# Kernel tuning notes

Hardware: AMD Instinct MI355X
Metric: run time of the kernel (lower is better)

## Reference

```python
import jax, jax.numpy as jnp
import numpy as np

EPS = 1e-7
MAX_TANH = 1.0 - 1e-6  # clamp for arctanh stability


def _norm(v):
    # last-axis L2 norm, clamped away from zero
    return jnp.maximum(jnp.linalg.norm(v, axis=-1, keepdims=True), EPS)


def log_map_zero(y):
    # Poincare ball (c=1) log map at the origin
    n = _norm(y)
    return jnp.arctanh(jnp.clip(n, 0.0, MAX_TANH)) * y / n


def exp_map_zero(v):
    # Poincare ball (c=1) exp map at the origin
    n = _norm(v)
    return jnp.tanh(n) * v / n


def h_add(x, y):
    # Mobius addition x (+) y on the Poincare ball (c=1)
    xy = jnp.sum(x * y, axis=-1, keepdims=True)
    x2 = jnp.sum(x * x, axis=-1, keepdims=True)
    y2 = jnp.sum(y * y, axis=-1, keepdims=True)
    num = (1.0 + 2.0 * xy + y2) * x + (1.0 - x2) * y
    den = 1.0 + 2.0 * xy + x2 * y2
    return num / jnp.maximum(den, EPS)


def h_mul(x, W):
    # Mobius matrix-vector multiply: exp0( log0(x) @ W )
    return exp_map_zero(log_map_zero(x) @ W)


def setup_inputs() -> dict:
    key = jax.random.key(0)
    k1, k2, k3, k4 = jax.random.split(key, 4)
    N, F_IN, F_OUT = 8192, 128, 128
    # node features inside the unit ball: ||x|| ~ 0.05*sqrt(128) ~ 0.57
    x = 0.05 * jax.random.normal(k1, (N, F_IN), dtype=jnp.float32)
    # sparse-ish row-normalized dense adjacency
    a = (jax.random.uniform(k2, (N, N)) < 0.01).astype(jnp.float32)
    adj = a / jnp.maximum(a.sum(axis=1, keepdims=True), 1.0)
    # xavier-uniform-ish weights
    lim_e = np.sqrt(6.0 / (F_IN + F_IN)) * np.sqrt(2.0)
    lim_l = np.sqrt(6.0 / (2 * F_IN + F_OUT)) * np.sqrt(2.0)
    embed = jax.random.uniform(k3, (F_IN, F_IN), minval=-lim_e, maxval=lim_e, dtype=jnp.float32)
    layer = jax.random.uniform(k4, (2 * F_IN, F_OUT), minval=-lim_l, maxval=lim_l, dtype=jnp.float32)
    embed_bias = jnp.zeros((F_IN,), dtype=jnp.float32)
    layer_bias = jnp.zeros((F_OUT,), dtype=jnp.float32)
    return {"x": x, "adj": adj, "embed": embed, "layer": layer,
            "embed_bias": embed_bias, "layer_bias": layer_bias}


def reference(x, adj, embed, layer, embed_bias, layer_bias):
    # h = (embed (x)mobius x) (+) embed_bias
    h = h_mul(x, embed)                      # [N, F_IN]
    h = h_add(h, embed_bias[None, :])
    # neighbor aggregation in tangent space at origin
    neigh = exp_map_zero(adj @ log_map_zero(h))   # [N, F_IN]
    # out = (layer (x)mobius [x ; neigh]) (+) layer_bias
    out = h_mul(jnp.concatenate((x, neigh), axis=1), layer)  # [N, F_OUT]
    out = h_add(out, layer_bias[None, :])
    return out
```

## Files before the change

kernel.cpp:

```cpp
#include <hip/hip_runtime.h>
#include <math.h>

#define EPS  1e-7f
#define MAXT 0.999999f

typedef short  s16x8  __attribute__((ext_vector_type(8)));
typedef float  f32x16 __attribute__((ext_vector_type(16)));

__device__ __forceinline__ float waveRedSum(float v) {
    #pragma unroll
    for (int off = 32; off > 0; off >>= 1)
        v += __shfl_xor(v, off, 64);
    return v;
}

__device__ __forceinline__ unsigned short f2bf(float f) {
    unsigned u = __float_as_uint(f);
    u += 0x7fff + ((u >> 16) & 1);
    return (unsigned short)(u >> 16);
}

__global__ __launch_bounds__(256) void kA(const float* __restrict__ x,
                                          const float* __restrict__ embed,
                                          const float* __restrict__ ebias,
                                          unsigned short* __restrict__ vpack) {
    __shared__ float u[4][128];
    const int wave = threadIdx.x >> 6;
    const int lane = threadIdx.x & 63;
    const int row  = blockIdx.x * 4 + wave;
    const int c0   = lane * 2;

    const float2 xr = *(const float2*)(x + (size_t)row * 128 + c0);

    float n2 = waveRedSum(xr.x * xr.x + xr.y * xr.y);
    float n  = fmaxf(sqrtf(n2), EPS);
    float sc = atanhf(fminf(n, MAXT)) / n;
    u[wave][c0]     = xr.x * sc;
    u[wave][c0 + 1] = xr.y * sc;
    __syncthreads();

    float a0 = 0.f, a1 = 0.f;
    #pragma unroll 8
    for (int k = 0; k < 128; k++) {
        float  uk = u[wave][k];
        float2 e  = *(const float2*)(embed + (size_t)k * 128 + c0);
        a0 = fmaf(uk, e.x, a0);
        a1 = fmaf(uk, e.y, a1);
    }

    float np2 = waveRedSum(a0 * a0 + a1 * a1);
    float np  = fmaxf(sqrtf(np2), EPS);
    float se  = tanhf(np) / np;
    float h0 = a0 * se, h1 = a1 * se;
    float x2 = np2 * se * se;

    float bx = ebias[c0], by = ebias[c0 + 1];
    float xy = waveRedSum(h0 * bx + h1 * by);
    float y2 = waveRedSum(bx * bx + by * by);
    float den = fmaxf(1.f + 2.f * xy + x2 * y2, EPS);
    float cx = 1.f + 2.f * xy + y2;
    float cy = 1.f - x2;
    float hb0 = (cx * h0 + cy * bx) / den;
    float hb1 = (cx * h1 + cy * by) / den;

    float m2 = waveRedSum(hb0 * hb0 + hb1 * hb1);
    float m  = fmaxf(sqrtf(m2), EPS);
    float sl = atanhf(fminf(m, MAXT)) / m;
    float v0 = hb0 * sl, v1 = hb1 * sl;

    const int tbase = (row >> 4) * 2048 + (row & 15);
    vpack[tbase + c0 * 16]       = f2bf(v0);
    vpack[tbase + (c0 + 1) * 16] = f2bf(v1);
}

#define BK 128

__global__ __launch_bounds__(256) void kB(const float* __restrict__ adj,
                                          const unsigned short* __restrict__ vpack,
                                          float* __restrict__ tpart,
                                          int klen) {
    __shared__ __align__(16) unsigned short As[32][BK + 8];

    const int tid  = threadIdx.x;
    const int wave = tid >> 6;
    const int lane = tid & 63;
    const int r0   = blockIdx.x * 32;
    const int k0   = blockIdx.y * klen;
    float* tout    = tpart + (size_t)blockIdx.y * 8192 * 128;

    const int srow = tid >> 3;
    const int scol = (tid & 7) * 16;
    const float* aptr = adj + (size_t)(r0 + srow) * 8192 + k0 + scol;

    const int m  = lane & 31;
    const int kh = lane >> 5;
    const int n  = wave * 32 + m;
    const unsigned short* vb = vpack + (size_t)n * 16 + kh * 8;

    f32x16 acc = {0.f};

    float4 f0 = *(const float4*)(aptr + 0);
    float4 f1 = *(const float4*)(aptr + 4);
    float4 f2 = *(const float4*)(aptr + 8);
    float4 f3 = *(const float4*)(aptr + 12);

    const int kiters = klen / BK;
    for (int it = 0; it < kiters; it++) {
        __syncthreads();

        union { unsigned short u[8]; s16x8 v; } p0, p1;
        p0.u[0] = f2bf(f0.x); p0.u[1] = f2bf(f0.y); p0.u[2] = f2bf(f0.z); p0.u[3] = f2bf(f0.w);
        p0.u[4] = f2bf(f1.x); p0.u[5] = f2bf(f1.y); p0.u[6] = f2bf(f1.z); p0.u[7] = f2bf(f1.w);
        p1.u[0] = f2bf(f2.x); p1.u[1] = f2bf(f2.y); p1.u[2] = f2bf(f2.z); p1.u[3] = f2bf(f2.w);
        p1.u[4] = f2bf(f3.x); p1.u[5] = f2bf(f3.y); p1.u[6] = f2bf(f3.z); p1.u[7] = f2bf(f3.w);
        *(s16x8*)&As[srow][scol]     = p0.v;
        *(s16x8*)&As[srow][scol + 8] = p1.v;
        __syncthreads();

        if (it + 1 < kiters) {
            aptr += BK;
            f0 = *(const float4*)(aptr + 0);
            f1 = *(const float4*)(aptr + 4);
            f2 = *(const float4*)(aptr + 8);
            f3 = *(const float4*)(aptr + 12);
        }

        const int ktile0 = (k0 + it * BK) >> 4;
        #pragma unroll
        for (int kk = 0; kk < BK / 16; kk++) {
            s16x8 a = *(const s16x8*)&As[m][kk * 16 + kh * 8];
            s16x8 b = *(const s16x8*)(vb + (size_t)(ktile0 + kk) * 2048);
            acc = __builtin_amdgcn_mfma_f32_32x32x16_bf16(a, b, acc, 0, 0, 0);
        }
    }

    #pragma unroll
    for (int r = 0; r < 16; r++) {
        int row = r0 + (r & 3) + 8 * (r >> 2) + 4 * kh;
        tout[(size_t)row * 128 + n] = acc[r];
    }
}

__global__ __launch_bounds__(256) void kC(const float* __restrict__ x,
                                          const float* __restrict__ tpart,
                                          const float* __restrict__ layer,
                                          const float* __restrict__ lbias,
                                          float* __restrict__ out,
                                          int S) {
    __shared__ float w[4][256];
    const int wave = threadIdx.x >> 6;
    const int lane = threadIdx.x & 63;
    const int row  = blockIdx.x * 4 + wave;
    const int c0   = lane * 2;

    float2 tr = *(const float2*)(tpart + (size_t)row * 128 + c0);
    for (int s = 1; s < S; s++) {
        float2 p = *(const float2*)(tpart + (size_t)s * 8192 * 128 + (size_t)row * 128 + c0);
        tr.x += p.x; tr.y += p.y;
    }
    const float2 xr = *(const float2*)(x + (size_t)row * 128 + c0);

    float st = waveRedSum(tr.x * tr.x + tr.y * tr.y);
    float sx = waveRedSum(xr.x * xr.x + xr.y * xr.y);

    float nt = fmaxf(sqrtf(st), EPS);
    float se = tanhf(nt) / nt;

    float ncat2 = sx + st * se * se;
    float ncat  = fmaxf(sqrtf(ncat2), EPS);
    float sw    = atanhf(fminf(ncat, MAXT)) / ncat;
    w[wave][c0]           = xr.x * sw;
    w[wave][c0 + 1]       = xr.y * sw;
    w[wave][128 + c0]     = tr.x * se * sw;
    w[wave][128 + c0 + 1] = tr.y * se * sw;
    __syncthreads();

    float a0 = 0.f, a1 = 0.f;
    #pragma unroll 8
    for (int k = 0; k < 256; k++) {
        float  wk = w[wave][k];
        float2 e  = *(const float2*)(layer + (size_t)k * 128 + c0);
        a0 = fmaf(wk, e.x, a0);
        a1 = fmaf(wk, e.y, a1);
    }

    float np2 = waveRedSum(a0 * a0 + a1 * a1);
    float np  = fmaxf(sqrtf(np2), EPS);
    float so  = tanhf(np) / np;
    float o0 = a0 * so, o1 = a1 * so;
    float x2 = np2 * so * so;

    float bx = lbias[c0], by = lbias[c0 + 1];
    float xy = waveRedSum(o0 * bx + o1 * by);
    float y2 = waveRedSum(bx * bx + by * by);
    float den = fmaxf(1.f + 2.f * xy + x2 * y2, EPS);
    float cx = 1.f + 2.f * xy + y2;
    float cy = 1.f - x2;

    float2 res;
    res.x = (cx * o0 + cy * bx) / den;
    res.y = (cx * o1 + cy * by) / den;
    *(float2*)(out + (size_t)row * 128 + c0) = res;
}

extern "C" void kernel_launch(void* const* d_in, const int* in_sizes, int n_in,
                              void* d_out, int out_size, void* d_ws, size_t ws_size,
                              hipStream_t stream) {
    const float* x     = (const float*)d_in[0];
    const float* adj   = (const float*)d_in[1];
    const float* embed = (const float*)d_in[2];
    const float* layer = (const float*)d_in[3];
    const float* eb    = (const float*)d_in[4];
    const float* lb    = (const float*)d_in[5];
    float* out = (float*)d_out;

    const size_t vbytes = (size_t)8192 * 128 * 2;
    const size_t slice  = (size_t)8192 * 128 * 4;

    int S = 1;
    if      (ws_size >= vbytes + 8 * slice) S = 8;
    else if (ws_size >= vbytes + 4 * slice) S = 4;
    else if (ws_size >= vbytes + 2 * slice) S = 2;

    unsigned short* vpack = (unsigned short*)d_ws;
    float* tpart = (float*)((char*)d_ws + vbytes);

    kA<<<2048, 256, 0, stream>>>(x, embed, eb, vpack);
    kB<<<dim3(256, S), 256, 0, stream>>>(adj, vpack, tpart, 8192 / S);
    kC<<<2048, 256, 0, stream>>>(x, tpart, layer, lb, out, S);
}
```

Baseline: 498.3 us.

## Fuse three stages into one cooperative persistent kernel with grid syncs

Replaces the three separate launches with a single cooperative kernel of 1024 blocks that runs the embed projection, the bf16 MFMA adjacency GEMM with a fixed 4-way K split, and the output projection, separated by grid-wide syncs. Each block processes two rows per wave in the elementwise stages so that embed and layer weight loads are reused. The aim is to remove launch gaps between stages. In exchange the GEMM has fewer K splits than the previous up-to-8, so less parallelism, and grid.sync carries its own overhead. A fallback to the old three-kernel path with S=8 runs if the cooperative launch fails; that fallback assumes the workspace holds 8 slices without checking ws_size.

Measured after the change: 709.8 us. 42.4% more time.

```diff
diff --git a/kernel.cpp b/kernel.cpp
--- a/kernel.cpp
+++ b/kernel.cpp
@@ -1,8 +1,11 @@
 #include <hip/hip_runtime.h>
+#include <hip/hip_cooperative_groups.h>
 #include <math.h>
 
 #define EPS  1e-7f
 #define MAXT 0.999999f
+
+namespace cg = cooperative_groups;
 
 typedef short  s16x8  __attribute__((ext_vector_type(8)));
 typedef float  f32x16 __attribute__((ext_vector_type(16)));
@@ -18,6 +21,196 @@
     unsigned u = __float_as_uint(f);
     u += 0x7fff + ((u >> 16) & 1);
     return (unsigned short)(u >> 16);
+}
+
+__device__ __forceinline__ void tangent_pack(float a0, float a1, float bx, float by,
+                                             float y2, int row, int c0,
+                                             unsigned short* __restrict__ vpack) {
+    float np2 = waveRedSum(a0*a0 + a1*a1);
+    float np  = fmaxf(sqrtf(np2), EPS);
+    float se  = tanhf(np)/np;
+    float h0 = a0*se, h1 = a1*se;
+    float x2 = np2*se*se;
+    float xy = waveRedSum(h0*bx + h1*by);
+    float den = fmaxf(1.f + 2.f*xy + x2*y2, EPS);
+    float cx = 1.f + 2.f*xy + y2;
+    float cy = 1.f - x2;
+    float hb0 = (cx*h0 + cy*bx)/den, hb1 = (cx*h1 + cy*by)/den;
+    float m2 = waveRedSum(hb0*hb0 + hb1*hb1);
+    float mm = fmaxf(sqrtf(m2), EPS);
+    float sl = atanhf(fminf(mm, MAXT))/mm;
+    const int tbase = (row >> 4)*2048 + (row & 15);
+    vpack[tbase + c0*16]       = f2bf(hb0*sl);
+    vpack[tbase + (c0+1)*16]   = f2bf(hb1*sl);
+}
+
+__device__ __forceinline__ void final_out(float a0, float a1, float bx, float by,
+                                          float y2, int row, int c0,
+                                          float* __restrict__ out) {
+    float np2 = waveRedSum(a0*a0 + a1*a1);
+    float np  = fmaxf(sqrtf(np2), EPS);
+    float so  = tanhf(np)/np;
+    float o0 = a0*so, o1 = a1*so;
+    float x2 = np2*so*so;
+    float xy = waveRedSum(o0*bx + o1*by);
+    float den = fmaxf(1.f + 2.f*xy + x2*y2, EPS);
+    float cx = 1.f + 2.f*xy + y2;
+    float cy = 1.f - x2;
+    float2 res;
+    res.x = (cx*o0 + cy*bx)/den;
+    res.y = (cx*o1 + cy*by)/den;
+    *(float2*)(out + (size_t)row*128 + c0) = res;
+}
+
+#define BK     128
+#define SPLITS 4
+#define KLEN   2048
+#define NBLK   1024
+
+__global__ __launch_bounds__(256, 4) void kFused(
+        const float* __restrict__ x, const float* __restrict__ adj,
+        const float* __restrict__ embed, const float* __restrict__ layer,
+        const float* __restrict__ eb, const float* __restrict__ lb,
+        float* __restrict__ out, unsigned short* __restrict__ vpack,
+        float* __restrict__ tpart)
+{
+    __shared__ __align__(16) char smraw[32*(BK+8)*2];
+    const int tid  = threadIdx.x;
+    const int wave = tid >> 6;
+    const int lane = tid & 63;
+    const int c0   = lane*2;
+    cg::grid_group grid = cg::this_grid();
+
+    {
+        float (*u)[2][128] = (float(*)[2][128])smraw;
+        const int row0 = blockIdx.x*8 + wave;
+        float2 xr0 = *(const float2*)(x + (size_t)row0*128 + c0);
+        float2 xr1 = *(const float2*)(x + (size_t)(row0+4)*128 + c0);
+        float n20 = waveRedSum(xr0.x*xr0.x + xr0.y*xr0.y);
+        float n21 = waveRedSum(xr1.x*xr1.x + xr1.y*xr1.y);
+        float nn0 = fmaxf(sqrtf(n20), EPS), nn1 = fmaxf(sqrtf(n21), EPS);
+        float s0 = atanhf(fminf(nn0, MAXT))/nn0;
+        float s1 = atanhf(fminf(nn1, MAXT))/nn1;
+        u[wave][0][c0] = xr0.x*s0; u[wave][0][c0+1] = xr0.y*s0;
+        u[wave][1][c0] = xr1.x*s1; u[wave][1][c0+1] = xr1.y*s1;
+        __syncthreads();
+        float a00=0.f, a01=0.f, a10=0.f, a11=0.f;
+        #pragma unroll 8
+        for (int k = 0; k < 128; k++) {
+            float uk0 = u[wave][0][k], uk1 = u[wave][1][k];
+            float2 e  = *(const float2*)(embed + (size_t)k*128 + c0);
+            a00 = fmaf(uk0, e.x, a00); a01 = fmaf(uk0, e.y, a01);
+            a10 = fmaf(uk1, e.x, a10); a11 = fmaf(uk1, e.y, a11);
+        }
+        float bx = eb[c0], by = eb[c0+1];
+        float y2 = waveRedSum(bx*bx + by*by);
+        tangent_pack(a00, a01, bx, by, y2, row0,     c0, vpack);
+        tangent_pack(a10, a11, bx, by, y2, row0 + 4, c0, vpack);
+    }
+
+    grid.sync();
+
+    {
+        unsigned short (*As)[BK+8] = (unsigned short(*)[BK+8])smraw;
+        const int bx = blockIdx.x & 255;
+        const int by = blockIdx.x >> 8;
+        const int r0 = bx*32;
+        const int k0 = by*KLEN;
+        float* tout  = tpart + (size_t)by * 8192 * 128;
+
+        const int srow = tid >> 3;
+        const int scol = (tid & 7) * 16;
+        const float* aptr = adj + (size_t)(r0 + srow)*8192 + k0 + scol;
+
+        const int m  = lane & 31;
+        const int kh = lane >> 5;
+        const int n  = wave*32 + m;
+        const unsigned short* vb = vpack + (size_t)n*16 + kh*8;
+
+        f32x16 acc = {0.f};
+
+        float4 f0 = *(const float4*)(aptr + 0);
+        float4 f1 = *(const float4*)(aptr + 4);
+        float4 f2 = *(const float4*)(aptr + 8);
+        float4 f3 = *(const float4*)(aptr + 12);
+
+        const int kiters = KLEN / BK;
+        for (int it = 0; it < kiters; it++) {
+            __syncthreads();
+            union { unsigned short u[8]; s16x8 v; } p0, p1;
+            p0.u[0]=f2bf(f0.x); p0.u[1]=f2bf(f0.y); p0.u[2]=f2bf(f0.z); p0.u[3]=f2bf(f0.w);
+            p0.u[4]=f2bf(f1.x); p0.u[5]=f2bf(f1.y); p0.u[6]=f2bf(f1.z); p0.u[7]=f2bf(f1.w);
+            p1.u[0]=f2bf(f2.x); p1.u[1]=f2bf(f2.y); p1.u[2]=f2bf(f2.z); p1.u[3]=f2bf(f2.w);
+            p1.u[4]=f2bf(f3.x); p1.u[5]=f2bf(f3.y); p1.u[6]=f2bf(f3.z); p1.u[7]=f2bf(f3.w);
+            *(s16x8*)&As[srow][scol]     = p0.v;
+            *(s16x8*)&As[srow][scol + 8] = p1.v;
+            __syncthreads();
+
+            if (it + 1 < kiters) {
+                aptr += BK;
+                f0 = *(const float4*)(aptr + 0);
+                f1 = *(const float4*)(aptr + 4);
+                f2 = *(const float4*)(aptr + 8);
+                f3 = *(const float4*)(aptr + 12);
+            }
+
+            const int ktile0 = (k0 + it*BK) >> 4;
+            #pragma unroll
+            for (int kk = 0; kk < BK/16; kk++) {
+                s16x8 a = *(const s16x8*)&As[m][kk*16 + kh*8];
+                s16x8 b = *(const s16x8*)(vb + (size_t)(ktile0 + kk)*2048);
+                acc = __builtin_amdgcn_mfma_f32_32x32x16_bf16(a, b, acc, 0, 0, 0);
+            }
+        }
+
+        #pragma unroll
+        for (int r = 0; r < 16; r++) {
+            int row = r0 + (r & 3) + 8*(r >> 2) + 4*kh;
+            tout[(size_t)row*128 + n] = acc[r];
+        }
+    }
+
+    grid.sync();
+
+    {
+        float (*w)[2][256] = (float(*)[2][256])smraw;
+        const int row0 = blockIdx.x*8 + wave;
+        #pragma unroll
+        for (int r = 0; r < 2; r++) {
+            const int row = row0 + 4*r;
+            float2 tr = *(const float2*)(tpart + (size_t)row*128 + c0);
+            #pragma unroll
+            for (int s = 1; s < SPLITS; s++) {
+                float2 p = *(const float2*)(tpart + (size_t)s*8192*128 + (size_t)row*128 + c0);
+                tr.x += p.x; tr.y += p.y;
+            }
+            const float2 xr = *(const float2*)(x + (size_t)row*128 + c0);
+            float st = waveRedSum(tr.x*tr.x + tr.y*tr.y);
+            float sx = waveRedSum(xr.x*xr.x + xr.y*xr.y);
+            float nt = fmaxf(sqrtf(st), EPS);
+            float se = tanhf(nt)/nt;
+            float ncat2 = sx + st*se*se;
+            float ncat  = fmaxf(sqrtf(ncat2), EPS);
+            float sw    = atanhf(fminf(ncat, MAXT))/ncat;
+            w[wave][r][c0]           = xr.x*sw;
+            w[wave][r][c0+1]         = xr.y*sw;
+            w[wave][r][128 + c0]     = tr.x*se*sw;
+            w[wave][r][128 + c0+1]   = tr.y*se*sw;
+        }
+        __syncthreads();
+        float a00=0.f, a01=0.f, a10=0.f, a11=0.f;
+        #pragma unroll 8
+        for (int k = 0; k < 256; k++) {
+            float wk0 = w[wave][0][k], wk1 = w[wave][1][k];
+            float2 e  = *(const float2*)(layer + (size_t)k*128 + c0);
+            a00 = fmaf(wk0, e.x, a00); a01 = fmaf(wk0, e.y, a01);
+            a10 = fmaf(wk1, e.x, a10); a11 = fmaf(wk1, e.y, a11);
+        }
+        float bx = lb[c0], by = lb[c0+1];
+        float y2 = waveRedSum(bx*bx + by*by);
+        final_out(a00, a01, bx, by, y2, row0,     c0, out);
+        final_out(a10, a11, bx, by, y2, row0 + 4, c0, out);
+    }
 }
 
 __global__ __launch_bounds__(256) void kA(const float* __restrict__ x,
@@ -31,7 +224,6 @@
     const int c0   = lane * 2;
 
     const float2 xr = *(const float2*)(x + (size_t)row * 128 + c0);
-
     float n2 = waveRedSum(xr.x * xr.x + xr.y * xr.y);
     float n  = fmaxf(sqrtf(n2), EPS);
     float sc = atanhf(fminf(n, MAXT)) / n;
@@ -47,40 +239,16 @@
         a0 = fmaf(uk, e.x, a0);
         a1 = fmaf(uk, e.y, a1);
     }
-
-    float np2 = waveRedSum(a0 * a0 + a1 * a1);
-    float np  = fmaxf(sqrtf(np2), EPS);
-    float se  = tanhf(np) / np;
-    float h0 = a0 * se, h1 = a1 * se;
-    float x2 = np2 * se * se;
-
     float bx = ebias[c0], by = ebias[c0 + 1];
-    float xy = waveRedSum(h0 * bx + h1 * by);
-    float y2 = waveRedSum(bx * bx + by * by);
-    float den = fmaxf(1.f + 2.f * xy + x2 * y2, EPS);
-    float cx = 1.f + 2.f * xy + y2;
-    float cy = 1.f - x2;
-    float hb0 = (cx * h0 + cy * bx) / den;
-    float hb1 = (cx * h1 + cy * by) / den;
-
-    float m2 = waveRedSum(hb0 * hb0 + hb1 * hb1);
-    float m  = fmaxf(sqrtf(m2), EPS);
-    float sl = atanhf(fminf(m, MAXT)) / m;
-    float v0 = hb0 * sl, v1 = hb1 * sl;
-
-    const int tbase = (row >> 4) * 2048 + (row & 15);
-    vpack[tbase + c0 * 16]       = f2bf(v0);
-    vpack[tbase + (c0 + 1) * 16] = f2bf(v1);
-}
-
-#define BK 128
+    float y2 = waveRedSum(bx*bx + by*by);
+    tangent_pack(a0, a1, bx, by, y2, row, c0, vpack);
+}
 
 __global__ __launch_bounds__(256) void kB(const float* __restrict__ adj,
                                           const unsigned short* __restrict__ vpack,
                                           float* __restrict__ tpart,
                                           int klen) {
     __shared__ __align__(16) unsigned short As[32][BK + 8];
-
     const int tid  = threadIdx.x;
     const int wave = tid >> 6;
     const int lane = tid & 63;
@@ -98,7 +266,6 @@
     const unsigned short* vb = vpack + (size_t)n * 16 + kh * 8;
 
     f32x16 acc = {0.f};
-
     float4 f0 = *(const float4*)(aptr + 0);
     float4 f1 = *(const float4*)(aptr + 4);
     float4 f2 = *(const float4*)(aptr + 8);
@@ -107,12 +274,11 @@
     const int kiters = klen / BK;
     for (int it = 0; it < kiters; it++) {
         __syncthreads();
-
         union { unsigned short u[8]; s16x8 v; } p0, p1;
-        p0.u[0] = f2bf(f0.x); p0.u[1] = f2bf(f0.y); p0.u[2] = f2bf(f0.z); p0.u[3] = f2bf(f0.w);
-        p0.u[4] = f2bf(f1.x); p0.u[5] = f2bf(f1.y); p0.u[6] = f2bf(f1.z); p0.u[7] = f2bf(f1.w);
-        p1.u[0] = f2bf(f2.x); p1.u[1] = f2bf(f2.y); p1.u[2] = f2bf(f2.z); p1.u[3] = f2bf(f2.w);
-        p1.u[4] = f2bf(f3.x); p1.u[5] = f2bf(f3.y); p1.u[6] = f2bf(f3.z); p1.u[7] = f2bf(f3.w);
+        p0.u[0]=f2bf(f0.x); p0.u[1]=f2bf(f0.y); p0.u[2]=f2bf(f0.z); p0.u[3]=f2bf(f0.w);
+        p0.u[4]=f2bf(f1.x); p0.u[5]=f2bf(f1.y); p0.u[6]=f2bf(f1.z); p0.u[7]=f2bf(f1.w);
+        p1.u[0]=f2bf(f2.x); p1.u[1]=f2bf(f2.y); p1.u[2]=f2bf(f2.z); p1.u[3]=f2bf(f2.w);
+        p1.u[4]=f2bf(f3.x); p1.u[5]=f2bf(f3.y); p1.u[6]=f2bf(f3.z); p1.u[7]=f2bf(f3.w);
         *(s16x8*)&As[srow][scol]     = p0.v;
         *(s16x8*)&As[srow][scol + 8] = p1.v;
         __syncthreads();
@@ -133,7 +299,6 @@
             acc = __builtin_amdgcn_mfma_f32_32x32x16_bf16(a, b, acc, 0, 0, 0);
         }
     }
-
     #pragma unroll
     for (int r = 0; r < 16; r++) {
         int row = r0 + (r & 3) + 8 * (r >> 2) + 4 * kh;
@@ -159,13 +324,10 @@
         tr.x += p.x; tr.y += p.y;
     }
     const float2 xr = *(const float2*)(x + (size_t)row * 128 + c0);
-
     float st = waveRedSum(tr.x * tr.x + tr.y * tr.y);
     float sx = waveRedSum(xr.x * xr.x + xr.y * xr.y);
-
     float nt = fmaxf(sqrtf(st), EPS);
     float se = tanhf(nt) / nt;
-
     float ncat2 = sx + st * se * se;
     float ncat  = fmaxf(sqrtf(ncat2), EPS);
     float sw    = atanhf(fminf(ncat, MAXT)) / ncat;
@@ -183,24 +345,9 @@
         a0 = fmaf(wk, e.x, a0);
         a1 = fmaf(wk, e.y, a1);
     }
-
-    float np2 = waveRedSum(a0 * a0 + a1 * a1);
-    float np  = fmaxf(sqrtf(np2), EPS);
-    float so  = tanhf(np) / np;
-    float o0 = a0 * so, o1 = a1 * so;
-    float x2 = np2 * so * so;
-
     float bx = lbias[c0], by = lbias[c0 + 1];
-    float xy = waveRedSum(o0 * bx + o1 * by);
     float y2 = waveRedSum(bx * bx + by * by);
-    float den = fmaxf(1.f + 2.f * xy + x2 * y2, EPS);
-    float cx = 1.f + 2.f * xy + y2;
-    float cy = 1.f - x2;
-
-    float2 res;
-    res.x = (cx * o0 + cy * bx) / den;
-    res.y = (cx * o1 + cy * by) / den;
-    *(float2*)(out + (size_t)row * 128 + c0) = res;
+    final_out(a0, a1, bx, by, y2, row, c0, out);
 }
 
 extern "C" void kernel_launch(void* const* d_in, const int* in_sizes, int n_in,
@@ -215,17 +362,18 @@
     float* out = (float*)d_out;
 
     const size_t vbytes = (size_t)8192 * 128 * 2;
-    const size_t slice  = (size_t)8192 * 128 * 4;
-
-    int S = 1;
-    if      (ws_size >= vbytes + 8 * slice) S = 8;
-    else if (ws_size >= vbytes + 4 * slice) S = 4;
-    else if (ws_size >= vbytes + 2 * slice) S = 2;
-
     unsigned short* vpack = (unsigned short*)d_ws;
     float* tpart = (float*)((char*)d_ws + vbytes);
 
-    kA<<<2048, 256, 0, stream>>>(x, embed, eb, vpack);
-    kB<<<dim3(256, S), 256, 0, stream>>>(adj, vpack, tpart, 8192 / S);
-    kC<<<2048, 256, 0, stream>>>(x, tpart, layer, lb, out, S);
-}
+    void* args[] = { (void*)&x, (void*)&adj, (void*)&embed, (void*)&layer,
+                     (void*)&eb, (void*)&lb, (void*)&out, (void*)&vpack, (void*)&tpart };
+
+    hipError_t err = hipLaunchCooperativeKernel(kFused, dim3(NBLK), dim3(256),
+                                                args, 0u, stream);
+    if (err != hipSuccess) {
+        const int S = 8;
+        kA<<<2048, 256, 0, stream>>>(x, embed, eb, vpack);
+        kB<<<dim3(256, S), 256, 0, stream>>>(adj, vpack, tpart, 8192 / S);
+        kC<<<2048, 256, 0, stream>>>(x, tpart, layer, lb, out, S);
+    }
+}
```

## Double-buffer adjacency tiles in LDS via async global-to-LDS copies

Applied to the files above, without the earlier changes.

The adjacency GEMM kernel now stages raw fp32 adj tiles into a double-buffered LDS array using global_load_lds async copies with an XOR swizzle. The next tile's copy is issued while MFMAs run on the current one, and bf16 conversion moves to the LDS read side. B fragments are prefetched into registers per iteration, launch bounds request 4 blocks per SM, and split-K is hardcoded to 8 regardless of workspace size. The remaining edits factor the epilogue math into helper functions. The change doubles LDS per block to 32KB, and forcing S=8 assumes the workspace is large enough.

Measured after the change: 488.9 us. Within noise of the previous version (-1.9%).

```diff
diff --git a/kernel.cpp b/kernel.cpp
--- a/kernel.cpp
+++ b/kernel.cpp
@@ -18,6 +18,52 @@
     unsigned u = __float_as_uint(f);
     u += 0x7fff + ((u >> 16) & 1);
     return (unsigned short)(u >> 16);
+}
+
+__device__ __forceinline__ void async_cp16(const float* src, void* ldsbase) {
+    __builtin_amdgcn_global_load_lds(
+        (const __attribute__((address_space(1))) unsigned int*)src,
+        (__attribute__((address_space(3))) unsigned int*)ldsbase,
+        16, 0, 0);
+}
+
+__device__ __forceinline__ void tangent_pack(float a0, float a1, float bx, float by,
+                                             float y2, int row, int c0,
+                                             unsigned short* __restrict__ vpack) {
+    float np2 = waveRedSum(a0*a0 + a1*a1);
+    float np  = fmaxf(sqrtf(np2), EPS);
+    float se  = tanhf(np)/np;
+    float h0 = a0*se, h1 = a1*se;
+    float x2 = np2*se*se;
+    float xy = waveRedSum(h0*bx + h1*by);
+    float den = fmaxf(1.f + 2.f*xy + x2*y2, EPS);
+    float cx = 1.f + 2.f*xy + y2;
+    float cy = 1.f - x2;
+    float hb0 = (cx*h0 + cy*bx)/den, hb1 = (cx*h1 + cy*by)/den;
+    float m2 = waveRedSum(hb0*hb0 + hb1*hb1);
+    float mm = fmaxf(sqrtf(m2), EPS);
+    float sl = atanhf(fminf(mm, MAXT))/mm;
+    const int tbase = (row >> 4)*2048 + (row & 15);
+    vpack[tbase + c0*16]       = f2bf(hb0*sl);
+    vpack[tbase + (c0+1)*16]   = f2bf(hb1*sl);
+}
+
+__device__ __forceinline__ void final_out(float a0, float a1, float bx, float by,
+                                          float y2, int row, int c0,
+                                          float* __restrict__ out) {
+    float np2 = waveRedSum(a0*a0 + a1*a1);
+    float np  = fmaxf(sqrtf(np2), EPS);
+    float so  = tanhf(np)/np;
+    float o0 = a0*so, o1 = a1*so;
+    float x2 = np2*so*so;
+    float xy = waveRedSum(o0*bx + o1*by);
+    float den = fmaxf(1.f + 2.f*xy + x2*y2, EPS);
+    float cx = 1.f + 2.f*xy + y2;
+    float cy = 1.f - x2;
+    float2 res;
+    res.x = (cx*o0 + cy*bx)/den;
+    res.y = (cx*o1 + cy*by)/den;
+    *(float2*)(out + (size_t)row*128 + c0) = res;
 }
 
 __global__ __launch_bounds__(256) void kA(const float* __restrict__ x,
@@ -31,7 +77,6 @@
     const int c0   = lane * 2;
 
     const float2 xr = *(const float2*)(x + (size_t)row * 128 + c0);
-
     float n2 = waveRedSum(xr.x * xr.x + xr.y * xr.y);
     float n  = fmaxf(sqrtf(n2), EPS);
     float sc = atanhf(fminf(n, MAXT)) / n;
@@ -47,40 +92,18 @@
         a0 = fmaf(uk, e.x, a0);
         a1 = fmaf(uk, e.y, a1);
     }
-
-    float np2 = waveRedSum(a0 * a0 + a1 * a1);
-    float np  = fmaxf(sqrtf(np2), EPS);
-    float se  = tanhf(np) / np;
-    float h0 = a0 * se, h1 = a1 * se;
-    float x2 = np2 * se * se;
-
     float bx = ebias[c0], by = ebias[c0 + 1];
-    float xy = waveRedSum(h0 * bx + h1 * by);
     float y2 = waveRedSum(bx * bx + by * by);
-    float den = fmaxf(1.f + 2.f * xy + x2 * y2, EPS);
-    float cx = 1.f + 2.f * xy + y2;
-    float cy = 1.f - x2;
-    float hb0 = (cx * h0 + cy * bx) / den;
-    float hb1 = (cx * h1 + cy * by) / den;
-
-    float m2 = waveRedSum(hb0 * hb0 + hb1 * hb1);
-    float m  = fmaxf(sqrtf(m2), EPS);
-    float sl = atanhf(fminf(m, MAXT)) / m;
-    float v0 = hb0 * sl, v1 = hb1 * sl;
-
-    const int tbase = (row >> 4) * 2048 + (row & 15);
-    vpack[tbase + c0 * 16]       = f2bf(v0);
-    vpack[tbase + (c0 + 1) * 16] = f2bf(v1);
+    tangent_pack(a0, a1, bx, by, y2, row, c0, vpack);
 }
 
 #define BK 128
 
-__global__ __launch_bounds__(256) void kB(const float* __restrict__ adj,
-                                          const unsigned short* __restrict__ vpack,
-                                          float* __restrict__ tpart,
-                                          int klen) {
-    __shared__ __align__(16) unsigned short As[32][BK + 8];
-
+__global__ __launch_bounds__(256, 4) void kB(const float* __restrict__ adj,
+                                             const unsigned short* __restrict__ vpack,
+                                             float* __restrict__ tpart,
+                                             int klen) {
+    __shared__ __align__(16) float Af[2][32][128];
     const int tid  = threadIdx.x;
     const int wave = tid >> 6;
     const int lane = tid & 63;
@@ -88,50 +111,59 @@
     const int k0   = blockIdx.y * klen;
     float* tout    = tpart + (size_t)blockIdx.y * 8192 * 128;
 
-    const int srow = tid >> 3;
-    const int scol = (tid & 7) * 16;
-    const float* aptr = adj + (size_t)(r0 + srow) * 8192 + k0 + scol;
+    const int rpar = lane >> 5;
+    const int cst  = lane & 31;
 
     const int m  = lane & 31;
     const int kh = lane >> 5;
     const int n  = wave * 32 + m;
+    const int sw = m & 7;
     const unsigned short* vb = vpack + (size_t)n * 16 + kh * 8;
 
     f32x16 acc = {0.f};
-
-    float4 f0 = *(const float4*)(aptr + 0);
-    float4 f1 = *(const float4*)(aptr + 4);
-    float4 f2 = *(const float4*)(aptr + 8);
-    float4 f3 = *(const float4*)(aptr + 12);
-
     const int kiters = klen / BK;
+
+    #pragma unroll
+    for (int j = 0; j < 4; j++) {
+        int i = wave * 4 + j;
+        int r = 2 * i + rpar;
+        const float* src = adj + (size_t)(r0 + r) * 8192 + k0 + ((cst ^ (r & 7)) << 2);
+        async_cp16(src, (char*)&Af[0][0][0] + i * 1024);
+    }
+    __syncthreads();
+
     for (int it = 0; it < kiters; it++) {
+        const int cur = it & 1;
+        const int ktile0 = (k0 + it * BK) >> 4;
+
+        s16x8 bfr[8];
+        #pragma unroll
+        for (int kk = 0; kk < 8; kk++)
+            bfr[kk] = *(const s16x8*)(vb + (size_t)(ktile0 + kk) * 2048);
+
+        if (it + 1 < kiters) {
+            #pragma unroll
+            for (int j = 0; j < 4; j++) {
+                int i = wave * 4 + j;
+                int r = 2 * i + rpar;
+                const float* src = adj + (size_t)(r0 + r) * 8192 + k0 + (it + 1) * BK
+                                 + ((cst ^ (r & 7)) << 2);
+                async_cp16(src, (char*)&Af[cur ^ 1][0][0] + i * 1024);
+            }
+        }
+
+        #pragma unroll
+        for (int kk = 0; kk < 8; kk++) {
+            const int q0 = kk * 4 + kh * 2;
+            const float4 lo = *(const float4*)&Af[cur][m][(q0 ^ sw) << 2];
+            const float4 hi = *(const float4*)&Af[cur][m][((q0 + 1) ^ sw) << 2];
+            union { unsigned short u[8]; s16x8 v; } p;
+            p.u[0] = f2bf(lo.x); p.u[1] = f2bf(lo.y); p.u[2] = f2bf(lo.z); p.u[3] = f2bf(lo.w);
+            p.u[4] = f2bf(hi.x); p.u[5] = f2bf(hi.y); p.u[6] = f2bf(hi.z); p.u[7] = f2bf(hi.w);
+            acc = __builtin_amdgcn_mfma_f32_32x32x16_bf16(p.v, bfr[kk], acc, 0, 0, 0);
+        }
+
         __syncthreads();
-
-        union { unsigned short u[8]; s16x8 v; } p0, p1;
-        p0.u[0] = f2bf(f0.x); p0.u[1] = f2bf(f0.y); p0.u[2] = f2bf(f0.z); p0.u[3] = f2bf(f0.w);
-        p0.u[4] = f2bf(f1.x); p0.u[5] = f2bf(f1.y); p0.u[6] = f2bf(f1.z); p0.u[7] = f2bf(f1.w);
-        p1.u[0] = f2bf(f2.x); p1.u[1] = f2bf(f2.y); p1.u[2] = f2bf(f2.z); p1.u[3] = f2bf(f2.w);
-        p1.u[4] = f2bf(f3.x); p1.u[5] = f2bf(f3.y); p1.u[6] = f2bf(f3.z); p1.u[7] = f2bf(f3.w);
-        *(s16x8*)&As[srow][scol]     = p0.v;
-        *(s16x8*)&As[srow][scol + 8] = p1.v;
-        __syncthreads();
-
-        if (it + 1 < kiters) {
-            aptr += BK;
-            f0 = *(const float4*)(aptr + 0);
-            f1 = *(const float4*)(aptr + 4);
-            f2 = *(const float4*)(aptr + 8);
-            f3 = *(const float4*)(aptr + 12);
-        }
-
-        const int ktile0 = (k0 + it * BK) >> 4;
-        #pragma unroll
-        for (int kk = 0; kk < BK / 16; kk++) {
-            s16x8 a = *(const s16x8*)&As[m][kk * 16 + kh * 8];
-            s16x8 b = *(const s16x8*)(vb + (size_t)(ktile0 + kk) * 2048);
-            acc = __builtin_amdgcn_mfma_f32_32x32x16_bf16(a, b, acc, 0, 0, 0);
-        }
     }
 
     #pragma unroll
@@ -159,13 +191,10 @@
         tr.x += p.x; tr.y += p.y;
     }
     const float2 xr = *(const float2*)(x + (size_t)row * 128 + c0);
-
     float st = waveRedSum(tr.x * tr.x + tr.y * tr.y);
     float sx = waveRedSum(xr.x * xr.x + xr.y * xr.y);
-
     float nt = fmaxf(sqrtf(st), EPS);
     float se = tanhf(nt) / nt;
-
     float ncat2 = sx + st * se * se;
     float ncat  = fmaxf(sqrtf(ncat2), EPS);
     float sw    = atanhf(fminf(ncat, MAXT)) / ncat;
@@ -183,24 +212,9 @@
         a0 = fmaf(wk, e.x, a0);
         a1 = fmaf(wk, e.y, a1);
     }
-
-    float np2 = waveRedSum(a0 * a0 + a1 * a1);
-    float np  = fmaxf(sqrtf(np2), EPS);
-    float so  = tanhf(np) / np;
-    float o0 = a0 * so, o1 = a1 * so;
-    float x2 = np2 * so * so;
-
     float bx = lbias[c0], by = lbias[c0 + 1];
-    float xy = waveRedSum(o0 * bx + o1 * by);
     float y2 = waveRedSum(bx * bx + by * by);
-    float den = fmaxf(1.f + 2.f * xy + x2 * y2, EPS);
-    float cx = 1.f + 2.f * xy + y2;
-    float cy = 1.f - x2;
-
-    float2 res;
-    res.x = (cx * o0 + cy * bx) / den;
-    res.y = (cx * o1 + cy * by) / den;
-    *(float2*)(out + (size_t)row * 128 + c0) = res;
+    final_out(a0, a1, bx, by, y2, row, c0, out);
 }
 
 extern "C" void kernel_launch(void* const* d_in, const int* in_sizes, int n_in,
@@ -215,16 +229,10 @@
     float* out = (float*)d_out;
 
     const size_t vbytes = (size_t)8192 * 128 * 2;
-    const size_t slice  = (size_t)8192 * 128 * 4;
-
-    int S = 1;
-    if      (ws_size >= vbytes + 8 * slice) S = 8;
-    else if (ws_size >= vbytes + 4 * slice) S = 4;
-    else if (ws_size >= vbytes + 2 * slice) S = 2;
-
     unsigned short* vpack = (unsigned short*)d_ws;
     float* tpart = (float*)((char*)d_ws + vbytes);
 
+    const int S = 8;
     kA<<<2048, 256, 0, stream>>>(x, embed, eb, vpack);
     kB<<<dim3(256, S), 256, 0, stream>>>(adj, vpack, tpart, 8192 / S);
     kC<<<2048, 256, 0, stream>>>(x, tpart, layer, lb, out, S);
```
